# Kernel tuning notes

Measured on AMD Instinct MI355X. Metric: run time of the kernel, lower is better.

Reference implementation:

```python
import jax, jax.numpy as jnp
import numpy as np

B, CIN, COUT, K, H, W = 4, 16, 16, 3, 128, 128


def setup_inputs() -> dict:
    key = jax.random.key(0)
    k1, k2, k3 = jax.random.split(key, 3)
    x = jax.random.normal(k1, (B, CIN, H, W), dtype=jnp.float32)
    # kaiming_uniform_(a=1.0): bound = sqrt(6 / ((1 + a^2) * fan_in)), fan_in = Cin*k*k
    fan_in = CIN * K * K
    bound = float(np.sqrt(6.0 / (2.0 * fan_in)))
    weights = jax.random.uniform(k2, (H, W, COUT, CIN, K, K), dtype=jnp.float32,
                                 minval=-bound, maxval=bound)
    bias = jax.random.normal(k3, (H, W, COUT), dtype=jnp.float32)
    return {"x": x, "weights": weights, "bias": bias}


def _xonv2d(x, weights, bias):
    b, c, h, w = x.shape
    k = weights.shape[-1]
    pad = k // 2
    if k % 2 == 1:
        xp = jnp.pad(x, ((0, 0), (0, 0), (pad, pad), (pad, pad)))
    else:
        xp = jnp.pad(x, ((0, 0), (0, 0), (pad - 1, pad), (pad - 1, pad)))
    # Unfold: patch element order matches torch view -> (c, kh, kw) flattened.
    # Stack k*k shifted views: (B, C, k*k, H, W)
    shifts = [xp[:, :, i:i + h, j:j + w] for i in range(k) for j in range(k)]
    patches = jnp.stack(shifts, axis=2)
    wflat = weights.reshape(h, w, weights.shape[2], c, k * k)  # (H,W,O,C,p)
    # out[b,o,h,w] = sum_{c,p} patches[b,c,p,h,w] * wflat[h,w,o,c,p]
    out = jnp.einsum('bcphw,hwocp->bohw', patches, wflat)
    out = out + jnp.transpose(bias, (2, 0, 1))[None]  # (1,O,H,W)
    return out


def reference(x, weights, bias):
    return _xonv2d(x, weights, bias)
```

## Files before the change

### kernel.cpp

```cpp
#include <hip/hip_runtime.h>


#define HWD  128
#define CIND 16
#define COUTD 16
#define BATCH 4

typedef float f4  __attribute__((ext_vector_type(4)));
typedef float f4u __attribute__((ext_vector_type(4), aligned(4)));

__global__ __launch_bounds__(256) void xonv2d_kernel(
    const float* __restrict__ x,
    const float* __restrict__ wts,
    const float* __restrict__ bias,
    float* __restrict__ out)
{
    __shared__ f4 wsm[4][576];

    const int lane = threadIdx.x & 63;
    const int wave = threadIdx.x >> 6;

    const int xcd = blockIdx.x & 7;
    const int idx = blockIdx.x >> 3;
    const int site = xcd * 2048 + idx * 4 + wave;
    const int h = site >> 7;
    const int w = site & 127;

    const int o = lane & 15;
    const int g = lane >> 4;
    const int c0 = g * 4;

    const f4* gw = (const f4*)wts + (size_t)site * 576;
    f4 st[9];
    #pragma unroll
    for (int j = 0; j < 9; ++j)
        st[j] = __builtin_nontemporal_load(gw + j * 64 + lane);

    const float bv = bias[(size_t)site * COUTD + o];

    #pragma unroll
    for (int j = 0; j < 9; ++j)
        wsm[wave][j * 64 + lane] = st[j];

    f4 wv[9];
    {
        const f4* lp = &wsm[wave][o * 36 + g * 9];
        #pragma unroll
        for (int j = 0; j < 9; ++j) wv[j] = lp[j];
    }
    const float* wf = (const float*)wv;

    float acc[BATCH] = {0.f, 0.f, 0.f, 0.f};

    const bool interior = (h >= 1) & (h <= HWD - 2) & (w >= 1) & (w <= HWD - 3);

    if (interior) {
        #pragma unroll
        for (int cc = 0; cc < 4; ++cc) {
            #pragma unroll
            for (int b = 0; b < BATCH; ++b) {
                const float* xb = x + (((size_t)(b * CIND + c0 + cc) * HWD + (h - 1)) * HWD) + (w - 1);
                f4 r0 = *(const f4u*)(xb);
                f4 r1 = *(const f4u*)(xb + HWD);
                f4 r2 = *(const f4u*)(xb + 2 * HWD);
                const float* wr = wf + cc * 9;
                acc[b] = fmaf(r0.x, wr[0], acc[b]);
                acc[b] = fmaf(r0.y, wr[1], acc[b]);
                acc[b] = fmaf(r0.z, wr[2], acc[b]);
                acc[b] = fmaf(r1.x, wr[3], acc[b]);
                acc[b] = fmaf(r1.y, wr[4], acc[b]);
                acc[b] = fmaf(r1.z, wr[5], acc[b]);
                acc[b] = fmaf(r2.x, wr[6], acc[b]);
                acc[b] = fmaf(r2.y, wr[7], acc[b]);
                acc[b] = fmaf(r2.z, wr[8], acc[b]);
            }
        }
    } else {
        #pragma unroll
        for (int cc = 0; cc < 4; ++cc) {
            #pragma unroll
            for (int b = 0; b < BATCH; ++b) {
                const float* xb = x + ((size_t)(b * CIND + c0 + cc)) * (HWD * HWD);
                #pragma unroll
                for (int kh = 0; kh < 3; ++kh) {
                    const int hy = h + kh - 1;
                    #pragma unroll
                    for (int kw = 0; kw < 3; ++kw) {
                        const int wx = w + kw - 1;
                        const bool ok = (hy >= 0) & (hy < HWD) & (wx >= 0) & (wx < HWD);
                        const float xv = ok ? xb[hy * HWD + wx] : 0.f;
                        acc[b] = fmaf(xv, wf[cc * 9 + kh * 3 + kw], acc[b]);
                    }
                }
            }
        }
    }

    float r[BATCH];
    #pragma unroll
    for (int b = 0; b < BATCH; ++b) {
        float v = acc[b];
        v += __shfl_xor(v, 32);
        v += __shfl_xor(v, 16);
        r[b] = v;
    }

    const float vout = (g == 0) ? r[0] : (g == 1) ? r[1] : (g == 2) ? r[2] : r[3];
    out[((size_t)(g * COUTD + o)) * (HWD * HWD) + h * HWD + w] = vout + bv;
}

extern "C" void kernel_launch(void* const* d_in, const int* in_sizes, int n_in,
                              void* d_out, int out_size, void* d_ws, size_t ws_size,
                              hipStream_t stream) {
    const float* x    = (const float*)d_in[0];
    const float* wts  = (const float*)d_in[1];
    const float* bias = (const float*)d_in[2];
    float* out = (float*)d_out;

    const int blocks = (HWD * HWD) / 4;
    xonv2d_kernel<<<blocks, 256, 0, stream>>>(x, wts, bias, out);
}
```

Baseline: 224.9 us.

## Double-buffer per-site weights via direct global-to-LDS loads across sites per wave

```diff
diff --git a/kernel.cpp b/kernel.cpp
--- a/kernel.cpp
+++ b/kernel.cpp
@@ -1,112 +1,135 @@
 #include <hip/hip_runtime.h>
 
 
-#define HWD  128
-#define CIND 16
+#define HWD   128
+#define CIND  16
 #define COUTD 16
 #define BATCH 4
+#define SPW   8
+#define WPB   2
 
 typedef float f4  __attribute__((ext_vector_type(4)));
 typedef float f4u __attribute__((ext_vector_type(4), aligned(4)));
 
-__global__ __launch_bounds__(256) void xonv2d_kernel(
+__device__ __forceinline__ void gload_lds16(const f4* gsrc, f4* ldst) {
+    __builtin_amdgcn_global_load_lds(
+        (const __attribute__((address_space(1))) unsigned int*)gsrc,
+        (__attribute__((address_space(3))) unsigned int*)ldst,
+        16, 0, 0);
+}
+
+__global__ __launch_bounds__(128) void xonv2d_kernel(
     const float* __restrict__ x,
     const float* __restrict__ wts,
     const float* __restrict__ bias,
     float* __restrict__ out)
 {
-    __shared__ f4 wsm[4][576];
+    __shared__ f4 wsm[WPB][2][576];
 
     const int lane = threadIdx.x & 63;
     const int wave = threadIdx.x >> 6;
 
     const int xcd = blockIdx.x & 7;
     const int idx = blockIdx.x >> 3;
-    const int site = xcd * 2048 + idx * 4 + wave;
-    const int h = site >> 7;
-    const int w = site & 127;
+    const int site0 = xcd * 2048 + (idx * WPB + wave) * SPW;
 
-    const int o = lane & 15;
-    const int g = lane >> 4;
+    const int o  = lane & 15;
+    const int g  = lane >> 4;
     const int c0 = g * 4;
 
-    const f4* gw = (const f4*)wts + (size_t)site * 576;
-    f4 st[9];
-    #pragma unroll
-    for (int j = 0; j < 9; ++j)
-        st[j] = __builtin_nontemporal_load(gw + j * 64 + lane);
+    {
+        const f4* gw = (const f4*)wts + (size_t)site0 * 576;
+        #pragma unroll
+        for (int j = 0; j < 9; ++j)
+            gload_lds16(gw + j * 64 + lane, &wsm[wave][0][j * 64]);
+    }
 
-    const float bv = bias[(size_t)site * COUTD + o];
+    int cur = 0;
+    #pragma unroll 1
+    for (int s = 0; s < SPW; ++s) {
+        const int site = site0 + s;
+        const int h = site >> 7;
+        const int w = site & 127;
 
-    #pragma unroll
-    for (int j = 0; j < 9; ++j)
-        wsm[wave][j * 64 + lane] = st[j];
+        asm volatile("s_waitcnt vmcnt(0)" ::: "memory");
 
-    f4 wv[9];
-    {
-        const f4* lp = &wsm[wave][o * 36 + g * 9];
-        #pragma unroll
-        for (int j = 0; j < 9; ++j) wv[j] = lp[j];
-    }
-    const float* wf = (const float*)wv;
+        if (s + 1 < SPW) {
+            const f4* gw = (const f4*)wts + (size_t)(site + 1) * 576;
+            #pragma unroll
+            for (int j = 0; j < 9; ++j)
+                gload_lds16(gw + j * 64 + lane, &wsm[wave][cur ^ 1][j * 64]);
+        }
 
-    float acc[BATCH] = {0.f, 0.f, 0.f, 0.f};
+        const float bv = bias[(size_t)site * COUTD + o];
 
-    const bool interior = (h >= 1) & (h <= HWD - 2) & (w >= 1) & (w <= HWD - 3);
+        f4 wv[9];
+        {
+            const f4* lp = &wsm[wave][cur][o * 36 + g * 9];
+            #pragma unroll
+            for (int j = 0; j < 9; ++j) wv[j] = lp[j];
+        }
+        const float* wf = (const float*)wv;
 
-    if (interior) {
-        #pragma unroll
-        for (int cc = 0; cc < 4; ++cc) {
+        float acc[BATCH] = {0.f, 0.f, 0.f, 0.f};
+
+        const bool interior = (h >= 1) & (h <= HWD - 2) & (w >= 1) & (w <= HWD - 3);
+
+        if (interior) {
             #pragma unroll
-            for (int b = 0; b < BATCH; ++b) {
-                const float* xb = x + (((size_t)(b * CIND + c0 + cc) * HWD + (h - 1)) * HWD) + (w - 1);
-                f4 r0 = *(const f4u*)(xb);
-                f4 r1 = *(const f4u*)(xb + HWD);
-                f4 r2 = *(const f4u*)(xb + 2 * HWD);
-                const float* wr = wf + cc * 9;
-                acc[b] = fmaf(r0.x, wr[0], acc[b]);
-                acc[b] = fmaf(r0.y, wr[1], acc[b]);
-                acc[b] = fmaf(r0.z, wr[2], acc[b]);
-                acc[b] = fmaf(r1.x, wr[3], acc[b]);
-                acc[b] = fmaf(r1.y, wr[4], acc[b]);
-                acc[b] = fmaf(r1.z, wr[5], acc[b]);
-                acc[b] = fmaf(r2.x, wr[6], acc[b]);
-                acc[b] = fmaf(r2.y, wr[7], acc[b]);
-                acc[b] = fmaf(r2.z, wr[8], acc[b]);
+            for (int cc = 0; cc < 4; ++cc) {
+                #pragma unroll
+                for (int b = 0; b < BATCH; ++b) {
+                    const float* xb = x + (((size_t)(b * CIND + c0 + cc) * HWD + (h - 1)) * HWD) + (w - 1);
+                    f4 r0 = *(const f4u*)(xb);
+                    f4 r1 = *(const f4u*)(xb + HWD);
+                    f4 r2 = *(const f4u*)(xb + 2 * HWD);
+                    const float* wr = wf + cc * 9;
+                    acc[b] = fmaf(r0.x, wr[0], acc[b]);
+                    acc[b] = fmaf(r0.y, wr[1], acc[b]);
+                    acc[b] = fmaf(r0.z, wr[2], acc[b]);
+                    acc[b] = fmaf(r1.x, wr[3], acc[b]);
+                    acc[b] = fmaf(r1.y, wr[4], acc[b]);
+                    acc[b] = fmaf(r1.z, wr[5], acc[b]);
+                    acc[b] = fmaf(r2.x, wr[6], acc[b]);
+                    acc[b] = fmaf(r2.y, wr[7], acc[b]);
+                    acc[b] = fmaf(r2.z, wr[8], acc[b]);
+                }
             }
-        }
-    } else {
-        #pragma unroll
-        for (int cc = 0; cc < 4; ++cc) {
+        } else {
             #pragma unroll
-            for (int b = 0; b < BATCH; ++b) {
-                const float* xb = x + ((size_t)(b * CIND + c0 + cc)) * (HWD * HWD);
+            for (int cc = 0; cc < 4; ++cc) {
                 #pragma unroll
-                for (int kh = 0; kh < 3; ++kh) {
-                    const int hy = h + kh - 1;
+                for (int b = 0; b < BATCH; ++b) {
+                    const float* xb = x + ((size_t)(b * CIND + c0 + cc)) * (HWD * HWD);
                     #pragma unroll
-                    for (int kw = 0; kw < 3; ++kw) {
-                        const int wx = w + kw - 1;
-                        const bool ok = (hy >= 0) & (hy < HWD) & (wx >= 0) & (wx < HWD);
-                        const float xv = ok ? xb[hy * HWD + wx] : 0.f;
-                        acc[b] = fmaf(xv, wf[cc * 9 + kh * 3 + kw], acc[b]);
+                    for (int kh = 0; kh < 3; ++kh) {
+                        const int hy = h + kh - 1;
+                        #pragma unroll
+                        for (int kw = 0; kw < 3; ++kw) {
+                            const int wx = w + kw - 1;
+                            const bool ok = (hy >= 0) & (hy < HWD) & (wx >= 0) & (wx < HWD);
+                            const float xv = ok ? xb[hy * HWD + wx] : 0.f;
+                            acc[b] = fmaf(xv, wf[cc * 9 + kh * 3 + kw], acc[b]);
+                        }
                     }
                 }
             }
         }
+
+        float r[BATCH];
+        #pragma unroll
+        for (int b = 0; b < BATCH; ++b) {
+            float v = acc[b];
+            v += __shfl_xor(v, 32);
+            v += __shfl_xor(v, 16);
+            r[b] = v;
+        }
+
+        const float vout = (g == 0) ? r[0] : (g == 1) ? r[1] : (g == 2) ? r[2] : r[3];
+        out[((size_t)(g * COUTD + o)) * (HWD * HWD) + h * HWD + w] = vout + bv;
+
+        cur ^= 1;
     }
-
-    float r[BATCH];
-    #pragma unroll
-    for (int b = 0; b < BATCH; ++b) {
-        float v = acc[b];
-        v += __shfl_xor(v, 32);
-        v += __shfl_xor(v, 16);
-        r[b] = v;
-    }
-
-    const float vout = (g == 0) ? r[0] : (g == 1) ? r[1] : (g == 2) ? r[2] : r[3];
-    out[((size_t)(g * COUTD + o)) * (HWD * HWD) + h * HWD + w] = vout + bv;
 }
 
 extern "C" void kernel_launch(void* const* d_in, const int* in_sizes, int n_in,
@@ -117,6 +140,6 @@
     const float* bias = (const float*)d_in[2];
     float* out = (float*)d_out;
 
-    const int blocks = (HWD * HWD) / 4;
-    xonv2d_kernel<<<blocks, 256, 0, stream>>>(x, wts, bias, out);
+    const int blocks = (HWD * HWD) / (WPB * SPW);
+    xonv2d_kernel<<<blocks, WPB * 64, 0, stream>>>(x, wts, bias, out);
 }
```

Measured after the change: 238.2 us. 5.9% more time.
